# Kernel optimization log

Hardware: AMD Instinct MI355X
Metric: run time of the kernel (lower is better)

## Reference

```python
import jax, jax.numpy as jnp
import numpy as np

B, N, D = 4, 2048, 1024
WIN, K, ALPHA = 4, 8, 0.3


def setup_inputs() -> dict:
    key = jax.random.key(0)
    ks = jax.random.split(key, 16)
    s_d = 1.0 / np.sqrt(D)
    s_2d = 1.0 / np.sqrt(2 * D)
    inp = {
        'mu': jax.random.normal(ks[0], (B, N, D), jnp.float32),
        'pheromone': jax.random.uniform(ks[1], (B, N), jnp.float32),
        'Wq': jax.random.normal(ks[2], (D, D), jnp.float32) * s_d,
        'bq': jnp.zeros((D,), jnp.float32),
        'Wk': jax.random.normal(ks[3], (D, D), jnp.float32) * s_d,
        'bk': jnp.zeros((D,), jnp.float32),
        'Wv': jax.random.normal(ks[4], (D, D), jnp.float32) * s_d,
        'bv': jnp.zeros((D,), jnp.float32),
        'Wm1': jax.random.normal(ks[5], (2 * D, D), jnp.float32) * s_2d,
        'bm1': jnp.zeros((D,), jnp.float32),
        'Wm2': jax.random.normal(ks[6], (D, D), jnp.float32) * s_d,
        'bm2': jnp.zeros((D,), jnp.float32),
        'Wo': jax.random.normal(ks[7], (2 * D, D), jnp.float32) * s_2d,
        'bo': jnp.zeros((D,), jnp.float32),
    }
    return inp


def reference(mu, pheromone, Wq, bq, Wk, bk, Wv, bv, Wm1, bm1, Wm2, bm2, Wo, bo):
    # ---- local windowed gather-MLP ----
    padded = jnp.pad(mu, ((0, 0), (WIN, 0), (0, 0)))  # causal left-pad
    neighbors = jnp.stack([padded[:, WIN - w:WIN - w + N, :] for w in range(1, WIN + 1)], axis=2)
    self_exp = jnp.broadcast_to(mu[:, :, None, :], neighbors.shape)
    cat = jnp.concatenate([self_exp, neighbors], axis=-1)
    h = jax.nn.silu(cat @ Wm1 + bm1) @ Wm2 + bm2
    local_msgs = h.mean(axis=2)  # (B,N,D)

    # ---- causal top-k attention with pheromone bias ----
    q = mu @ Wq + bq
    k = mu @ Wk + bk
    v = mu @ Wv + bv
    scale = 1.0 / jnp.sqrt(jnp.asarray(D, mu.dtype))
    scores = jnp.einsum('bnd,bmd->bnm', q, k) * scale  # (B,N,N)
    scores = scores + ALPHA * pheromone[:, None, :]
    row = jnp.arange(N)
    causal = jnp.where(row[None, :] > row[:, None], -jnp.inf, 0.0).astype(mu.dtype)
    scores = scores + causal[None]
    # top-k sparsification (N > K): softmax over the k kept scores, zeros elsewhere
    vals, idx = jax.lax.top_k(scores, K)  # (B,N,K)
    probs = jax.nn.softmax(vals, axis=-1)
    bi = jnp.arange(B)[:, None, None]
    ni = jnp.arange(N)[None, :, None]
    attn = jnp.zeros_like(scores).at[bi, ni, idx].set(probs)
    global_msgs = jnp.einsum('bnm,bmd->bnd', attn, v)

    return jnp.concatenate([local_msgs, global_msgs], axis=-1) @ Wo + bo
```

## Files before the change

kernel.cpp:

```cpp
#include <hip/hip_runtime.h>
#include <hip/hip_bf16.h>
#include <math.h>

#define B_ 4
#define N_ 2048
#define D_ 1024
#define WIN_ 4
#define KTOP 8
#define ALPHA_ 0.3f
#define SCALE_ (1.0f/32.0f)
#define NCH 16
#define TROW 36

typedef unsigned short ushortT;
typedef __attribute__((ext_vector_type(8))) short short8v;
typedef __attribute__((ext_vector_type(4))) float f32x4;

__device__ inline ushortT f2b(float f) {
    unsigned int u = __float_as_uint(f);
    unsigned int r = (u + 0x7fffu + ((u >> 16) & 1u)) >> 16;
    return (ushortT)r;
}
__device__ inline float b2f(ushortT u) {
    return __uint_as_float(((unsigned int)u) << 16);
}

__global__ __launch_bounds__(256)
void split3_mu(const float* __restrict__ src, ushortT* __restrict__ Pa,
               ushortT* __restrict__ Pb, ushortT* __restrict__ CCbase)
{
    size_t base = ((size_t)blockIdx.x * 256 + threadIdx.x) * 4;
    int row = (int)(base >> 10);
    int col = (int)(base & 1023);
    float4 v = *reinterpret_cast<const float4*>(&src[base]);
    ushort4 pa, pb, pc;
    float vv[4] = {v.x, v.y, v.z, v.w};
#pragma unroll
    for (int j = 0; j < 4; ++j) {
        float f = vv[j];
        ushortT a = f2b(f);  float r1 = f - b2f(a);
        ushortT b = f2b(r1); float r2 = r1 - b2f(b);
        ushortT c = f2b(r2);
        ((ushortT*)&pa)[j] = a; ((ushortT*)&pb)[j] = b; ((ushortT*)&pc)[j] = c;
    }
    *reinterpret_cast<ushort4*>(&Pa[base]) = pa;
    *reinterpret_cast<ushort4*>(&Pb[base]) = pb;
    *reinterpret_cast<ushort4*>(&CCbase[(size_t)row * 2048 + 1024 + col]) = pc;
}

__global__ __launch_bounds__(256)
void transpose_f2b(const float* __restrict__ W, ushortT* __restrict__ Wt,
                   int K, int Nn)
{
    __shared__ float t[32][33];
    const int k0 = blockIdx.x * 32, n0 = blockIdx.y * 32;
    const int tx = threadIdx.x & 31, ty8 = threadIdx.x >> 5;
#pragma unroll
    for (int p = 0; p < 4; ++p) {
        int kk = p * 8 + ty8;
        t[kk][tx] = W[(size_t)(k0 + kk) * Nn + n0 + tx];
    }
    __syncthreads();
#pragma unroll
    for (int p = 0; p < 4; ++p) {
        int nn = p * 8 + ty8;
        Wt[(size_t)(n0 + nn) * K + k0 + tx] = f2b(t[tx][nn]);
    }
}

__global__ __launch_bounds__(256)
void transpose_split3(const float* __restrict__ W, ushortT* __restrict__ Pa,
                      ushortT* __restrict__ Pb, ushortT* __restrict__ Pc,
                      int K, int Nn)
{
    __shared__ float t[32][33];
    const int k0 = blockIdx.x * 32, n0 = blockIdx.y * 32;
    const int tx = threadIdx.x & 31, ty8 = threadIdx.x >> 5;
#pragma unroll
    for (int p = 0; p < 4; ++p) {
        int kk = p * 8 + ty8;
        t[kk][tx] = W[(size_t)(k0 + kk) * Nn + n0 + tx];
    }
    __syncthreads();
#pragma unroll
    for (int p = 0; p < 4; ++p) {
        int nn = p * 8 + ty8;
        float f = t[tx][nn];
        ushortT a = f2b(f);  float r1 = f - b2f(a);
        ushortT b = f2b(r1); float r2 = r1 - b2f(b);
        ushortT c = f2b(r2);
        size_t o = (size_t)(n0 + nn) * K + k0 + tx;
        Pa[o] = a; Pb[o] = b; Pc[o] = c;
    }
}

template<int BF16OUT>
__global__ __launch_bounds__(256)
void mfma_gemm(const ushortT* __restrict__ A, int lda,
               const ushortT* __restrict__ Bt, int ldb,
               const float* __restrict__ bias,
               void* __restrict__ Cout, int ldc, int K)
{
    __shared__ ushortT AsL[128 * 72];
    __shared__ ushortT BsL[128 * 72];
    const int tid = threadIdx.x;
    const int m0 = blockIdx.y * 128;
    const int n0 = blockIdx.x * 128;
    const int w = tid >> 6, lane = tid & 63;
    const int wr = w >> 1, wc = w & 1;

    f32x4 acc[4][4];
#pragma unroll
    for (int mi = 0; mi < 4; ++mi)
#pragma unroll
        for (int ni = 0; ni < 4; ++ni) acc[mi][ni] = (f32x4){0.f, 0.f, 0.f, 0.f};

    for (int k0 = 0; k0 < K; k0 += 64) {
#pragma unroll
        for (int it = 0; it < 4; ++it) {
            int idx = tid + it * 256;
            int row = idx >> 3, c = idx & 7;
            int4 va = *reinterpret_cast<const int4*>(&A[(size_t)(m0 + row) * lda + k0 + c * 8]);
            *reinterpret_cast<int4*>(&AsL[row * 72 + c * 8]) = va;
            int4 vb = *reinterpret_cast<const int4*>(&Bt[(size_t)(n0 + row) * ldb + k0 + c * 8]);
            *reinterpret_cast<int4*>(&BsL[row * 72 + c * 8]) = vb;
        }
        __syncthreads();
#pragma unroll
        for (int kh = 0; kh < 2; ++kh) {
            const int ko = kh * 32 + (lane >> 4) * 8;
            const int rr = lane & 15;
            short8v af[4], bf[4];
#pragma unroll
            for (int mi = 0; mi < 4; ++mi)
                af[mi] = *reinterpret_cast<const short8v*>(&AsL[(wr * 64 + mi * 16 + rr) * 72 + ko]);
#pragma unroll
            for (int ni = 0; ni < 4; ++ni)
                bf[ni] = *reinterpret_cast<const short8v*>(&BsL[(wc * 64 + ni * 16 + rr) * 72 + ko]);
#pragma unroll
            for (int mi = 0; mi < 4; ++mi)
#pragma unroll
                for (int ni = 0; ni < 4; ++ni)
                    acc[mi][ni] = __builtin_amdgcn_mfma_f32_16x16x32_bf16(
                        af[mi], bf[ni], acc[mi][ni], 0, 0, 0);
        }
        __syncthreads();
    }

    const int r4 = (lane >> 4) * 4, cl = lane & 15;
#pragma unroll
    for (int mi = 0; mi < 4; ++mi)
#pragma unroll
        for (int ni = 0; ni < 4; ++ni) {
            int row = m0 + wr * 64 + mi * 16 + r4;
            int col = n0 + wc * 64 + ni * 16 + cl;
            float bb = bias ? bias[col] : 0.f;
#pragma unroll
            for (int r = 0; r < 4; ++r) {
                float v = acc[mi][ni][r] + bb;
                if (BF16OUT)
                    ((ushortT*)Cout)[(size_t)(row + r) * ldc + col] = f2b(v);
                else
                    ((float*)Cout)[(size_t)(row + r) * ldc + col] = v;
            }
        }
}

__global__ __launch_bounds__(256)
void silu_mean(const float* __restrict__ A, const float* __restrict__ Nb,
               ushortT* __restrict__ Sb)
{
    size_t idx4 = (size_t)blockIdx.x * blockDim.x + threadIdx.x;
    size_t base = idx4 << 2;
    int n = (int)((base >> 10) & (N_ - 1));
    float4 a = *reinterpret_cast<const float4*>(&A[base]);
    float sx = 0.f, sy = 0.f, sz = 0.f, sw = 0.f;
#pragma unroll
    for (int w = 1; w <= WIN_; ++w) {
        float xx = a.x, xy = a.y, xz = a.z, xw = a.w;
        if (n >= w) {
            const float4 nb = *reinterpret_cast<const float4*>(&Nb[base - (size_t)w * D_]);
            xx += nb.x; xy += nb.y; xz += nb.z; xw += nb.w;
        }
        sx += xx / (1.f + __expf(-xx));
        sy += xy / (1.f + __expf(-xy));
        sz += xz / (1.f + __expf(-xz));
        sw += xw / (1.f + __expf(-xw));
    }
    ushort4 o = {f2b(sx * 0.25f), f2b(sy * 0.25f), f2b(sz * 0.25f), f2b(sw * 0.25f)};
    *reinterpret_cast<ushort4*>(&Sb[base]) = o;
}

__device__ inline void topk_insert(float (&tv)[KTOP], int (&ti)[KTOP], float s, int m)
{
    if ((s > tv[KTOP-1]) || (s == tv[KTOP-1] && m < ti[KTOP-1])) {
        float cs = s; int ci = m;
#pragma unroll
        for (int q = 0; q < KTOP; ++q) {
            bool beats = (cs > tv[q]) || (cs == tv[q] && ci < ti[q]);
            if (beats) { float t0 = tv[q]; int t1 = ti[q];
                         tv[q] = cs; ti[q] = ci; cs = t0; ci = t1; }
        }
    }
}

#define SPLIT6_COMPUTE(T6, wr, wc, lane, acc)                                   \
    {                                                                           \
        const int rr_ = (lane) & 15, ko_ = ((lane) >> 4) * 8;                   \
        _Pragma("unroll")                                                       \
        for (int p_ = 0; p_ < 3; ++p_) {                                        \
            short8v aF_[4];                                                     \
            _Pragma("unroll")                                                   \
            for (int mi_ = 0; mi_ < 4; ++mi_)                                   \
                aF_[mi_] = *reinterpret_cast<const short8v*>(                   \
                    &T6[p_ * 4608 + ((wr) * 64 + mi_ * 16 + rr_) * TROW + ko_]);\
            _Pragma("unroll")                                                   \
            for (int q_ = 0; q_ < 3; ++q_) {                                    \
                if (p_ + q_ > 2) continue;                                      \
                short8v b0_ = *reinterpret_cast<const short8v*>(                \
                    &T6[(3 + q_) * 4608 + ((wc) * 32 + rr_) * TROW + ko_]);     \
                short8v b1_ = *reinterpret_cast<const short8v*>(                \
                    &T6[(3 + q_) * 4608 + ((wc) * 32 + 16 + rr_) * TROW + ko_]);\
                _Pragma("unroll")                                               \
                for (int mi_ = 0; mi_ < 4; ++mi_) {                             \
                    acc[mi_][0] = __builtin_amdgcn_mfma_f32_16x16x32_bf16(      \
                        aF_[mi_], b0_, acc[mi_][0], 0, 0, 0);                   \
                    acc[mi_][1] = __builtin_amdgcn_mfma_f32_16x16x32_bf16(      \
                        aF_[mi_], b1_, acc[mi_][1], 0, 0, 0);                   \
                }                                                               \
            }                                                                   \
        }                                                                       \
    }

__global__ __launch_bounds__(512, 4)
void gemm_split6(const ushortT* __restrict__ A0, const ushortT* __restrict__ A1,
                 const ushortT* __restrict__ A2, int lda, int ldac,
                 const ushortT* __restrict__ B0, const ushortT* __restrict__ B1,
                 const ushortT* __restrict__ B2,
                 const float* __restrict__ bias,
                 ushortT* __restrict__ Pa, ushortT* __restrict__ Pb,
                 ushortT* __restrict__ Pc)
{
    __shared__ ushortT T6[6 * 128 * TROW];

    int lin = blockIdx.y * 8 + blockIdx.x;
    lin = (lin & 7) * 64 + (lin >> 3);
    const int m0 = (lin >> 3) * 128;
    const int n0 = (lin & 7) * 128;

    const int tid = threadIdx.x;
    const int wid = tid >> 6, lane = tid & 63;
    const int wr = wid >> 2, wc = wid & 3;
    const int rowL = tid >> 2, cL = tid & 3;

    const size_t offA  = (size_t)(m0 + rowL) * lda + cL * 8;
    const size_t offAc = (size_t)(m0 + rowL) * ldac + cL * 8;
    const size_t offB  = (size_t)(n0 + rowL) * D_ + cL * 8;
    const int ldst = rowL * TROW + cL * 8;

    f32x4 acc[4][2];
#pragma unroll
    for (int mi = 0; mi < 4; ++mi) { acc[mi][0] = (f32x4){0,0,0,0}; acc[mi][1] = (f32x4){0,0,0,0}; }

    int4 s0, s1, s2, s3, s4, s5;
    s0 = *reinterpret_cast<const int4*>(&A0[offA]);
    s1 = *reinterpret_cast<const int4*>(&A1[offA]);
    s2 = *reinterpret_cast<const int4*>(&A2[offAc]);
    s3 = *reinterpret_cast<const int4*>(&B0[offB]);
    s4 = *reinterpret_cast<const int4*>(&B1[offB]);
    s5 = *reinterpret_cast<const int4*>(&B2[offB]);

    for (int ks = 0; ks < 32; ++ks) {
        __syncthreads();
        *reinterpret_cast<int4*>(&T6[0 * 4608 + ldst]) = s0;
        *reinterpret_cast<int4*>(&T6[1 * 4608 + ldst]) = s1;
        *reinterpret_cast<int4*>(&T6[2 * 4608 + ldst]) = s2;
        *reinterpret_cast<int4*>(&T6[3 * 4608 + ldst]) = s3;
        *reinterpret_cast<int4*>(&T6[4 * 4608 + ldst]) = s4;
        *reinterpret_cast<int4*>(&T6[5 * 4608 + ldst]) = s5;
        __syncthreads();
        if (ks < 31) {
            const int kk = (ks + 1) * 32;
            s0 = *reinterpret_cast<const int4*>(&A0[offA + kk]);
            s1 = *reinterpret_cast<const int4*>(&A1[offA + kk]);
            s2 = *reinterpret_cast<const int4*>(&A2[offAc + kk]);
            s3 = *reinterpret_cast<const int4*>(&B0[offB + kk]);
            s4 = *reinterpret_cast<const int4*>(&B1[offB + kk]);
            s5 = *reinterpret_cast<const int4*>(&B2[offB + kk]);
        }
        SPLIT6_COMPUTE(T6, wr, wc, lane, acc)
    }

    const int r4 = (lane >> 4) * 4, cl = lane & 15;
#pragma unroll
    for (int mi = 0; mi < 4; ++mi)
#pragma unroll
        for (int ni = 0; ni < 2; ++ni) {
            int col = n0 + wc * 32 + ni * 16 + cl;
            float bb = bias[col];
#pragma unroll
            for (int r = 0; r < 4; ++r) {
                int row = m0 + wr * 64 + mi * 16 + r4 + r;
                float v = acc[mi][ni][r] + bb;
                ushortT a = f2b(v);  float r1 = v - b2f(a);
                ushortT b = f2b(r1); float r2 = r1 - b2f(b);
                ushortT c = f2b(r2);
                size_t o = (size_t)row * D_ + col;
                Pa[o] = a; Pb[o] = b; Pc[o] = c;
            }
        }
}

__global__ __launch_bounds__(512, 4)
void attn_scores_mfma2(const ushortT* __restrict__ Qa, const ushortT* __restrict__ Qb2,
                       const ushortT* __restrict__ Qc,
                       const ushortT* __restrict__ Ka, const ushortT* __restrict__ Kb2,
                       const ushortT* __restrict__ Kc,
                       const float* __restrict__ pher,
                       float* __restrict__ WV, int* __restrict__ WI)
{
    __shared__ ushortT T6[6 * 128 * TROW];
    __shared__ float Ps[128];
    float* MV = reinterpret_cast<float*>(&T6[0]);
    int*   MI = reinterpret_cast<int*>((char*)&T6[0] + 16384);
    float* PV = reinterpret_cast<float*>((char*)&T6[0] + 32768);
    int*   PI = reinterpret_cast<int*>((char*)&T6[0] + 36864);

    int lin = blockIdx.y * 136 + blockIdx.x;
    lin = (lin & 7) * 68 + (lin >> 3);
    const int b = lin / 136;
    const int xy = lin - b * 136;
    int g = 0;
    while ((g + 1) * (g + 2) / 2 <= xy) ++g;
    const int ch = xy - g * (g + 1) / 2;
    const int n0 = g * 128;
    const int m0 = ch * 128;
    const size_t bN = (size_t)b * N_;

    const int tid = threadIdx.x;
    const int wid = tid >> 6, lane = tid & 63;
    const int wr = wid >> 2, wc = wid & 3;
    const int rowL = tid >> 2, cL = tid & 3;

    if (tid < 128) Ps[tid] = pher[bN + m0 + tid];

    const size_t offQ = (bN + n0 + rowL) * (size_t)D_ + cL * 8;
    const size_t offK = (bN + m0 + rowL) * (size_t)D_ + cL * 8;
    const int ldst = rowL * TROW + cL * 8;

    f32x4 acc[4][2];
#pragma unroll
    for (int mi = 0; mi < 4; ++mi) { acc[mi][0] = (f32x4){0,0,0,0}; acc[mi][1] = (f32x4){0,0,0,0}; }

    int4 s0, s1, s2, s3, s4, s5;
    s0 = *reinterpret_cast<const int4*>(&Qa[offQ]);
    s1 = *reinterpret_cast<const int4*>(&Qb2[offQ]);
    s2 = *reinterpret_cast<const int4*>(&Qc[offQ]);
    s3 = *reinterpret_cast<const int4*>(&Ka[offK]);
    s4 = *reinterpret_cast<const int4*>(&Kb2[offK]);
    s5 = *reinterpret_cast<const int4*>(&Kc[offK]);

    for (int ks = 0; ks < 32; ++ks) {
        __syncthreads();
        *reinterpret_cast<int4*>(&T6[0 * 4608 + ldst]) = s0;
        *reinterpret_cast<int4*>(&T6[1 * 4608 + ldst]) = s1;
        *reinterpret_cast<int4*>(&T6[2 * 4608 + ldst]) = s2;
        *reinterpret_cast<int4*>(&T6[3 * 4608 + ldst]) = s3;
        *reinterpret_cast<int4*>(&T6[4 * 4608 + ldst]) = s4;
        *reinterpret_cast<int4*>(&T6[5 * 4608 + ldst]) = s5;
        __syncthreads();
        if (ks < 31) {
            const int kk = (ks + 1) * 32;
            s0 = *reinterpret_cast<const int4*>(&Qa[offQ + kk]);
            s1 = *reinterpret_cast<const int4*>(&Qb2[offQ + kk]);
            s2 = *reinterpret_cast<const int4*>(&Qc[offQ + kk]);
            s3 = *reinterpret_cast<const int4*>(&Ka[offK + kk]);
            s4 = *reinterpret_cast<const int4*>(&Kb2[offK + kk]);
            s5 = *reinterpret_cast<const int4*>(&Kc[offK + kk]);
        }
        SPLIT6_COMPUTE(T6, wr, wc, lane, acc)
    }

    const int r4 = (lane >> 4) * 4, cl = lane & 15;
    for (int p = 0; p < 4; ++p) {
        __syncthreads();
        if (wr == (p >> 1)) {
#pragma unroll
            for (int mi2 = 0; mi2 < 2; ++mi2) {
                const int mi = (p & 1) * 2 + mi2;
#pragma unroll
                for (int ni = 0; ni < 2; ++ni) {
                    int col = wc * 32 + ni * 16 + cl;
                    int m = m0 + col;
#pragma unroll
                    for (int r = 0; r < 4; ++r) {
                        int rloc = mi2 * 16 + r4 + r;
                        int n = n0 + p * 32 + rloc;
                        bool ok = (m <= n);
                        MV[rloc * 128 + col] = ok ? (acc[mi][ni][r] * SCALE_ + ALPHA_ * Ps[col])
                                                  : -INFINITY;
                        MI[rloc * 128 + col] = ok ? m : 0x7fffffff;
                    }
                }
            }
        }
        __syncthreads();
        if (tid < 128) {
            const int row = tid >> 2, q4 = tid & 3;
            float tv[KTOP]; int ti[KTOP];
#pragma unroll
            for (int j = 0; j < KTOP; ++j) { tv[j] = -INFINITY; ti[j] = 0x7fffffff; }
            for (int j = 0; j < 32; ++j) {
                float s = MV[row * 128 + q4 * 32 + j];
                if (s == -INFINITY) continue;
                topk_insert(tv, ti, s, MI[row * 128 + q4 * 32 + j]);
            }
#pragma unroll
            for (int j = 0; j < KTOP; ++j) {
                PV[(row * 4 + q4) * 8 + j] = tv[j];
                PI[(row * 4 + q4) * 8 + j] = ti[j];
            }
        }
        __syncthreads();
        if (tid < 32) {
            float tv[KTOP]; int ti[KTOP];
#pragma unroll
            for (int j = 0; j < KTOP; ++j) { tv[j] = -INFINITY; ti[j] = 0x7fffffff; }
            for (int i = 0; i < 32; ++i) {
                float s = PV[tid * 32 + i];
                if (s == -INFINITY) continue;
                topk_insert(tv, ti, s, PI[tid * 32 + i]);
            }
            int n = n0 + p * 32 + tid;
            size_t base = ((bN + n) * NCH + ch) * 8;
#pragma unroll
            for (int j = 0; j < KTOP; ++j) { WV[base + j] = tv[j]; WI[base + j] = ti[j]; }
        }
    }
}

__global__ __launch_bounds__(256)
void attn_merge(const float* __restrict__ WV, const int* __restrict__ WI,
                const ushortT* __restrict__ V, ushortT* __restrict__ CCb)
{
    __shared__ float CV[4][128];
    __shared__ int   CI[4][128];
    __shared__ float Pp[4][KTOP];
    __shared__ int   Pi[4][KTOP];

    const int tid  = threadIdx.x;
    const int wv   = tid >> 6;
    const int lane = tid & 63;
    const int rid  = blockIdx.x * 4 + wv;
    const int b    = rid >> 11;
    const int n    = rid & (N_ - 1);
    const int ncand = ((n >> 7) + 1) * 8;
    const size_t cbase = (size_t)rid * (NCH * 8);

#pragma unroll
    for (int t = 0; t < 2; ++t) {
        int i = lane + t * 64;
        if (i < ncand) { CV[wv][i] = WV[cbase + i]; CI[wv][i] = WI[cbase + i]; }
        else           { CV[wv][i] = -INFINITY;     CI[wv][i] = 0x7fffffff;   }
    }
    __syncthreads();

    if (lane == 0) {
        float tv[KTOP]; int ti[KTOP];
#pragma unroll
        for (int j = 0; j < KTOP; ++j) { tv[j] = -INFINITY; ti[j] = 0x7fffffff; }
        for (int i = 0; i < 128; ++i) {
            float s = CV[wv][i];
            if (s == -INFINITY) continue;
            topk_insert(tv, ti, s, CI[wv][i]);
        }
        float mx = tv[0];
        float e[KTOP]; float sum = 0.f;
#pragma unroll
        for (int j = 0; j < KTOP; ++j) {
            e[j] = (tv[j] == -INFINITY) ? 0.f : __expf(tv[j] - mx);
            sum += e[j];
        }
        float inv = 1.f / sum;
#pragma unroll
        for (int j = 0; j < KTOP; ++j) {
            Pp[wv][j] = e[j] * inv;
            Pi[wv][j] = (tv[j] == -INFINITY) ? 0 : ti[j];
        }
    }
    __syncthreads();

    const size_t vbase = (size_t)b * N_ * D_;
#pragma unroll
    for (int it = 0; it < 2; ++it) {
        int c8 = (it * 64 + lane) * 8;
        float o[8];
#pragma unroll
        for (int u = 0; u < 8; ++u) o[u] = 0.f;
#pragma unroll
        for (int j = 0; j < KTOP; ++j) {
            float p = Pp[wv][j];
            ushort4 v0 = *reinterpret_cast<const ushort4*>(
                &V[vbase + (size_t)Pi[wv][j] * D_ + c8]);
            ushort4 v1 = *reinterpret_cast<const ushort4*>(
                &V[vbase + (size_t)Pi[wv][j] * D_ + c8 + 4]);
            o[0] = fmaf(p, b2f(v0.x), o[0]); o[1] = fmaf(p, b2f(v0.y), o[1]);
            o[2] = fmaf(p, b2f(v0.z), o[2]); o[3] = fmaf(p, b2f(v0.w), o[3]);
            o[4] = fmaf(p, b2f(v1.x), o[4]); o[5] = fmaf(p, b2f(v1.y), o[5]);
            o[6] = fmaf(p, b2f(v1.z), o[6]); o[7] = fmaf(p, b2f(v1.w), o[7]);
        }
        ushort4 ob0 = {f2b(o[0]), f2b(o[1]), f2b(o[2]), f2b(o[3])};
        ushort4 ob1 = {f2b(o[4]), f2b(o[5]), f2b(o[6]), f2b(o[7])};
        *reinterpret_cast<ushort4*>(&CCb[(size_t)rid * 2048 + 1024 + c8]) = ob0;
        *reinterpret_cast<ushort4*>(&CCb[(size_t)rid * 2048 + 1024 + c8 + 4]) = ob1;
    }
}

extern "C" void kernel_launch(void* const* d_in, const int* in_sizes, int n_in,
                              void* d_out, int out_size, void* d_ws, size_t ws_size,
                              hipStream_t stream)
{
    const float* mu   = (const float*)d_in[0];
    const float* pher = (const float*)d_in[1];
    const float* Wq   = (const float*)d_in[2];
    const float* bq   = (const float*)d_in[3];
    const float* Wk   = (const float*)d_in[4];
    const float* bk   = (const float*)d_in[5];
    const float* Wv   = (const float*)d_in[6];
    const float* bv   = (const float*)d_in[7];
    const float* Wm1  = (const float*)d_in[8];
    const float* bm1  = (const float*)d_in[9];
    const float* Wm2  = (const float*)d_in[10];
    const float* bm2  = (const float*)d_in[11];
    const float* Wo   = (const float*)d_in[12];
    const float* bo   = (const float*)d_in[13];
    float* out = (float*)d_out;
    float* ws  = (float*)d_ws;

    const size_t SZ  = (size_t)B_ * N_ * D_;
    const size_t MEG = 1024 * 1024;
    const int M = B_ * N_;

    ushortT* CCb   = (ushortT*)ws;
    ushortT* mu_cp = CCb + 1024;
    float*   AbF   = ws + SZ;
    ushortT* Qa    = (ushortT*)(ws + SZ);
    ushortT* Qb2   = Qa + SZ;
    float*   NbF   = ws + 2 * SZ;
    ushortT* Ka    = (ushortT*)(ws + 2 * SZ);
    ushortT* Kb2   = Ka + SZ;
    ushortT* mu_a  = (ushortT*)(ws + 3 * SZ);
    ushortT* mu_bp = (ushortT*)(ws + 3 * SZ + SZ / 2);
    float*   WVb   = (float*)(ws + 3 * SZ + SZ / 2);
    int*     WIb   = (int*)(WVb + MEG);
    ushortT* U     = (ushortT*)(ws + 4 * SZ);
    ushortT* Wt_m1 = U;
    ushortT* Wt_m2 = U + 2 * MEG;
    ushortT* Wt_v  = U + 3 * MEG;
    ushortT* WqT_a = U;            ushortT* WqT_b = U + MEG;     ushortT* WqT_c = U + 2 * MEG;
    ushortT* WkT_a = U + 3 * MEG;  ushortT* WkT_b = U + 4 * MEG; ushortT* WkT_c = U + 5 * MEG;
    ushortT* Wt_o  = U;
    ushortT* Vb16  = (ushortT*)(ws + 4 * SZ + 3 * MEG);
    ushortT* SbB   = (ushortT*)(ws + 4 * SZ + 3 * MEG + SZ / 2);
    ushortT* Qc    = SbB;
    ushortT* Kc    = (ushortT*)(ws + 4 * SZ + 3 * MEG + SZ);

    dim3 blk256(256), blk512(512);
    dim3 gD(8, 64);

    hipLaunchKernelGGL(split3_mu, dim3(SZ / 4 / 256), blk256, 0, stream, mu, mu_a, mu_bp, CCb);
    hipLaunchKernelGGL(transpose_f2b, dim3(64, 32), blk256, 0, stream, Wm1, Wt_m1, 2048, 1024);
    hipLaunchKernelGGL(transpose_f2b, dim3(32, 32), blk256, 0, stream, Wm2, Wt_m2, 1024, 1024);
    hipLaunchKernelGGL(transpose_f2b, dim3(32, 32), blk256, 0, stream, Wv, Wt_v, 1024, 1024);
    hipLaunchKernelGGL((mfma_gemm<0>), gD, blk256, 0, stream,
                       mu_a, D_, Wt_m1, 2048, bm1, (void*)AbF, D_, D_);
    hipLaunchKernelGGL((mfma_gemm<0>), gD, blk256, 0, stream,
                       mu_a, D_, Wt_m1 + 1024, 2048, (const float*)nullptr, (void*)NbF, D_, D_);
    hipLaunchKernelGGL(silu_mean, dim3(SZ / 4 / 256), blk256, 0, stream, AbF, NbF, SbB);
    hipLaunchKernelGGL((mfma_gemm<1>), gD, blk256, 0, stream,
                       SbB, D_, Wt_m2, D_, bm2, (void*)CCb, 2 * D_, D_);
    hipLaunchKernelGGL((mfma_gemm<1>), gD, blk256, 0, stream,
                       mu_a, D_, Wt_v, D_, bv, (void*)Vb16, D_, D_);
    hipLaunchKernelGGL(transpose_split3, dim3(32, 32), blk256, 0, stream,
                       Wq, WqT_a, WqT_b, WqT_c, 1024, 1024);
    hipLaunchKernelGGL(transpose_split3, dim3(32, 32), blk256, 0, stream,
                       Wk, WkT_a, WkT_b, WkT_c, 1024, 1024);
    hipLaunchKernelGGL(gemm_split6, gD, blk512, 0, stream,
                       mu_a, mu_bp, mu_cp, D_, 2 * D_,
                       WqT_a, WqT_b, WqT_c, bq, Qa, Qb2, Qc);
    hipLaunchKernelGGL(gemm_split6, gD, blk512, 0, stream,
                       mu_a, mu_bp, mu_cp, D_, 2 * D_,
                       WkT_a, WkT_b, WkT_c, bk, Ka, Kb2, Kc);
    hipLaunchKernelGGL(transpose_f2b, dim3(64, 32), blk256, 0, stream, Wo, Wt_o, 2048, 1024);
    hipLaunchKernelGGL(attn_scores_mfma2, dim3(136, B_), blk512, 0, stream,
                       Qa, Qb2, Qc, Ka, Kb2, Kc, pher, WVb, WIb);
    hipLaunchKernelGGL(attn_merge, dim3(M / 4), blk256, 0, stream, WVb, WIb, Vb16, CCb);
    hipLaunchKernelGGL((mfma_gemm<0>), gD, blk256, 0, stream,
                       CCb, 2 * D_, Wt_o, 2048, bo, (void*)out, D_, 2 * D_);

    (void)in_sizes; (void)n_in; (void)out_size; (void)ws_size;
}
```

Before: 896.1 us.

## Use 64x64 per-wave tiles with 256-thread blocks in split6 GEMM and scores

Both split-precision MFMA kernels (gemm_split6 and attn_scores_mfma2) move from 8 waves with 64x32 wave tiles to 4 waves with 64x64 wave tiles. Each thread now stages two 16-byte chunks per operand per k-step. The compute loop loads all three A-split fragments once and reuses each B fragment across four MFMA columns, which cuts LDS reads per MFMA. The cost is more accumulator and fragment registers per thread (launch bounds 256,2) and fewer waves to hide latency. The top-k epilogue must still be correct with half the threads.

```diff
diff --git a/kernel.cpp b/kernel.cpp
--- a/kernel.cpp
+++ b/kernel.cpp
@@ -204,35 +204,62 @@
     }
 }
 
-#define SPLIT6_COMPUTE(T6, wr, wc, lane, acc)                                   \
+#define SPLIT6_COMPUTE64(T6, wr, wc, lane, acc)                                 \
     {                                                                           \
         const int rr_ = (lane) & 15, ko_ = ((lane) >> 4) * 8;                   \
+        short8v aF_[3][4];                                                      \
         _Pragma("unroll")                                                       \
         for (int p_ = 0; p_ < 3; ++p_) {                                        \
-            short8v aF_[4];                                                     \
             _Pragma("unroll")                                                   \
             for (int mi_ = 0; mi_ < 4; ++mi_)                                   \
-                aF_[mi_] = *reinterpret_cast<const short8v*>(                   \
+                aF_[p_][mi_] = *reinterpret_cast<const short8v*>(               \
                     &T6[p_ * 4608 + ((wr) * 64 + mi_ * 16 + rr_) * TROW + ko_]);\
+        }                                                                       \
+        _Pragma("unroll")                                                       \
+        for (int q_ = 0; q_ < 3; ++q_) {                                        \
+            short8v bF_[4];                                                     \
             _Pragma("unroll")                                                   \
-            for (int q_ = 0; q_ < 3; ++q_) {                                    \
-                if (p_ + q_ > 2) continue;                                      \
-                short8v b0_ = *reinterpret_cast<const short8v*>(                \
-                    &T6[(3 + q_) * 4608 + ((wc) * 32 + rr_) * TROW + ko_]);     \
-                short8v b1_ = *reinterpret_cast<const short8v*>(                \
-                    &T6[(3 + q_) * 4608 + ((wc) * 32 + 16 + rr_) * TROW + ko_]);\
+            for (int ni_ = 0; ni_ < 4; ++ni_)                                   \
+                bF_[ni_] = *reinterpret_cast<const short8v*>(                   \
+                    &T6[(3 + q_) * 4608 + ((wc) * 64 + ni_ * 16 + rr_) * TROW + ko_]); \
+            _Pragma("unroll")                                                   \
+            for (int p_ = 0; p_ < 3 - q_; ++p_) {                               \
                 _Pragma("unroll")                                               \
-                for (int mi_ = 0; mi_ < 4; ++mi_) {                             \
-                    acc[mi_][0] = __builtin_amdgcn_mfma_f32_16x16x32_bf16(      \
-                        aF_[mi_], b0_, acc[mi_][0], 0, 0, 0);                   \
-                    acc[mi_][1] = __builtin_amdgcn_mfma_f32_16x16x32_bf16(      \
-                        aF_[mi_], b1_, acc[mi_][1], 0, 0, 0);                   \
-                }                                                               \
+                for (int mi_ = 0; mi_ < 4; ++mi_)                               \
+                    _Pragma("unroll")                                           \
+                    for (int ni_ = 0; ni_ < 4; ++ni_)                           \
+                        acc[mi_][ni_] = __builtin_amdgcn_mfma_f32_16x16x32_bf16(\
+                            aF_[p_][mi_], bF_[ni_], acc[mi_][ni_], 0, 0, 0);    \
             }                                                                   \
         }                                                                       \
     }
 
-__global__ __launch_bounds__(512, 4)
+#define SPLIT6_LOAD(sreg, P0, P1, P2, P3, P4, P5, oA, oAc, oB, kk)              \
+    {                                                                           \
+        sreg[0][0] = *reinterpret_cast<const int4*>(&P0[oA + (kk)]);            \
+        sreg[0][1] = *reinterpret_cast<const int4*>(&P0[oA + (kk) + 8]);        \
+        sreg[1][0] = *reinterpret_cast<const int4*>(&P1[oA + (kk)]);            \
+        sreg[1][1] = *reinterpret_cast<const int4*>(&P1[oA + (kk) + 8]);        \
+        sreg[2][0] = *reinterpret_cast<const int4*>(&P2[oAc + (kk)]);           \
+        sreg[2][1] = *reinterpret_cast<const int4*>(&P2[oAc + (kk) + 8]);       \
+        sreg[3][0] = *reinterpret_cast<const int4*>(&P3[oB + (kk)]);            \
+        sreg[3][1] = *reinterpret_cast<const int4*>(&P3[oB + (kk) + 8]);        \
+        sreg[4][0] = *reinterpret_cast<const int4*>(&P4[oB + (kk)]);            \
+        sreg[4][1] = *reinterpret_cast<const int4*>(&P4[oB + (kk) + 8]);        \
+        sreg[5][0] = *reinterpret_cast<const int4*>(&P5[oB + (kk)]);            \
+        sreg[5][1] = *reinterpret_cast<const int4*>(&P5[oB + (kk) + 8]);        \
+    }
+
+#define SPLIT6_STORE(sreg, ldst)                                                \
+    {                                                                           \
+        _Pragma("unroll")                                                       \
+        for (int t_ = 0; t_ < 6; ++t_) {                                        \
+            *reinterpret_cast<int4*>(&T6[t_ * 4608 + (ldst)]) = sreg[t_][0];    \
+            *reinterpret_cast<int4*>(&T6[t_ * 4608 + (ldst) + 8]) = sreg[t_][1];\
+        }                                                                       \
+    }
+
+__global__ __launch_bounds__(256, 2)
 void gemm_split6(const ushortT* __restrict__ A0, const ushortT* __restrict__ A1,
                  const ushortT* __restrict__ A2, int lda, int ldac,
                  const ushortT* __restrict__ B0, const ushortT* __restrict__ B1,
@@ -250,53 +277,41 @@
 
     const int tid = threadIdx.x;
     const int wid = tid >> 6, lane = tid & 63;
-    const int wr = wid >> 2, wc = wid & 3;
-    const int rowL = tid >> 2, cL = tid & 3;
-
-    const size_t offA  = (size_t)(m0 + rowL) * lda + cL * 8;
-    const size_t offAc = (size_t)(m0 + rowL) * ldac + cL * 8;
-    const size_t offB  = (size_t)(n0 + rowL) * D_ + cL * 8;
-    const int ldst = rowL * TROW + cL * 8;
-
-    f32x4 acc[4][2];
-#pragma unroll
-    for (int mi = 0; mi < 4; ++mi) { acc[mi][0] = (f32x4){0,0,0,0}; acc[mi][1] = (f32x4){0,0,0,0}; }
-
-    int4 s0, s1, s2, s3, s4, s5;
-    s0 = *reinterpret_cast<const int4*>(&A0[offA]);
-    s1 = *reinterpret_cast<const int4*>(&A1[offA]);
-    s2 = *reinterpret_cast<const int4*>(&A2[offAc]);
-    s3 = *reinterpret_cast<const int4*>(&B0[offB]);
-    s4 = *reinterpret_cast<const int4*>(&B1[offB]);
-    s5 = *reinterpret_cast<const int4*>(&B2[offB]);
+    const int wr = wid >> 1, wc = wid & 1;
+    const int rowL = tid >> 1;
+    const int cL2  = (tid & 1) * 16;
+
+    const size_t offA  = (size_t)(m0 + rowL) * lda + cL2;
+    const size_t offAc = (size_t)(m0 + rowL) * ldac + cL2;
+    const size_t offB  = (size_t)(n0 + rowL) * D_ + cL2;
+    const int ldst = rowL * TROW + cL2;
+
+    f32x4 acc[4][4];
+#pragma unroll
+    for (int mi = 0; mi < 4; ++mi)
+#pragma unroll
+        for (int ni = 0; ni < 4; ++ni) acc[mi][ni] = (f32x4){0,0,0,0};
+
+    int4 s[6][2];
+    SPLIT6_LOAD(s, A0, A1, A2, B0, B1, B2, offA, offAc, offB, 0)
 
     for (int ks = 0; ks < 32; ++ks) {
         __syncthreads();
-        *reinterpret_cast<int4*>(&T6[0 * 4608 + ldst]) = s0;
-        *reinterpret_cast<int4*>(&T6[1 * 4608 + ldst]) = s1;
-        *reinterpret_cast<int4*>(&T6[2 * 4608 + ldst]) = s2;
-        *reinterpret_cast<int4*>(&T6[3 * 4608 + ldst]) = s3;
-        *reinterpret_cast<int4*>(&T6[4 * 4608 + ldst]) = s4;
-        *reinterpret_cast<int4*>(&T6[5 * 4608 + ldst]) = s5;
+        SPLIT6_STORE(s, ldst)
         __syncthreads();
         if (ks < 31) {
             const int kk = (ks + 1) * 32;
-            s0 = *reinterpret_cast<const int4*>(&A0[offA + kk]);
-            s1 = *reinterpret_cast<const int4*>(&A1[offA + kk]);
-            s2 = *reinterpret_cast<const int4*>(&A2[offAc + kk]);
-            s3 = *reinterpret_cast<const int4*>(&B0[offB + kk]);
-            s4 = *reinterpret_cast<const int4*>(&B1[offB + kk]);
-            s5 = *reinterpret_cast<const int4*>(&B2[offB + kk]);
-        }
-        SPLIT6_COMPUTE(T6, wr, wc, lane, acc)
+            SPLIT6_LOAD(s, A0, A1, A2, B0, B1, B2, offA, offAc, offB, kk)
+        }
+        SPLIT6_COMPUTE64(T6, wr, wc, lane, acc)
     }
 
     const int r4 = (lane >> 4) * 4, cl = lane & 15;
 #pragma unroll
     for (int mi = 0; mi < 4; ++mi)
 #pragma unroll
-        for (int ni = 0; ni < 2; ++ni) {
-            int col = n0 + wc * 32 + ni * 16 + cl;
+        for (int ni = 0; ni < 4; ++ni) {
+            int col = n0 + wc * 64 + ni * 16 + cl;
             float bb = bias[col];
 #pragma unroll
             for (int r = 0; r < 4; ++r) {
@@ -311,7 +326,7 @@
         }
 }
 
-__global__ __launch_bounds__(512, 4)
+__global__ __launch_bounds__(256, 2)
 void attn_scores_mfma2(const ushortT* __restrict__ Qa, const ushortT* __restrict__ Qb2,
                        const ushortT* __restrict__ Qc,
                        const ushortT* __restrict__ Ka, const ushortT* __restrict__ Kb2,
@@ -339,46 +354,34 @@
 
     const int tid = threadIdx.x;
     const int wid = tid >> 6, lane = tid & 63;
-    const int wr = wid >> 2, wc = wid & 3;
-    const int rowL = tid >> 2, cL = tid & 3;
+    const int wr = wid >> 1, wc = wid & 1;
+    const int rowL = tid >> 1;
+    const int cL2  = (tid & 1) * 16;
 
     if (tid < 128) Ps[tid] = pher[bN + m0 + tid];
 
-    const size_t offQ = (bN + n0 + rowL) * (size_t)D_ + cL * 8;
-    const size_t offK = (bN + m0 + rowL) * (size_t)D_ + cL * 8;
-    const int ldst = rowL * TROW + cL * 8;
-
-    f32x4 acc[4][2];
-#pragma unroll
-    for (int mi = 0; mi < 4; ++mi) { acc[mi][0] = (f32x4){0,0,0,0}; acc[mi][1] = (f32x4){0,0,0,0}; }
-
-    int4 s0, s1, s2, s3, s4, s5;
-    s0 = *reinterpret_cast<const int4*>(&Qa[offQ]);
-    s1 = *reinterpret_cast<const int4*>(&Qb2[offQ]);
-    s2 = *reinterpret_cast<const int4*>(&Qc[offQ]);
-    s3 = *reinterpret_cast<const int4*>(&Ka[offK]);
-    s4 = *reinterpret_cast<const int4*>(&Kb2[offK]);
-    s5 = *reinterpret_cast<const int4*>(&Kc[offK]);
+    const size_t offQ = (bN + n0 + rowL) * (size_t)D_ + cL2;
+    const size_t offK = (bN + m0 + rowL) * (size_t)D_ + cL2;
+    const int ldst = rowL * TROW + cL2;
+
+    f32x4 acc[4][4];
+#pragma unroll
+    for (int mi = 0; mi < 4; ++mi)
+#pragma unroll
+        for (int ni = 0; ni < 4; ++ni) acc[mi][ni] = (f32x4){0,0,0,0};
+
+    int4 s[6][2];
+    SPLIT6_LOAD(s, Qa, Qb2, Qc, Ka, Kb2, Kc, offQ, offQ, offK, 0)
 
     for (int ks = 0; ks < 32; ++ks) {
         __syncthreads();
-        *reinterpret_cast<int4*>(&T6[0 * 4608 + ldst]) = s0;
-        *reinterpret_cast<int4*>(&T6[1 * 4608 + ldst]) = s1;
-        *reinterpret_cast<int4*>(&T6[2 * 4608 + ldst]) = s2;
-        *reinterpret_cast<int4*>(&T6[3 * 4608 + ldst]) = s3;
-        *reinterpret_cast<int4*>(&T6[4 * 4608 + ldst]) = s4;
-        *reinterpret_cast<int4*>(&T6[5 * 4608 + ldst]) = s5;
+        SPLIT6_STORE(s, ldst)
         __syncthreads();
         if (ks < 31) {
             const int kk = (ks + 1) * 32;
-            s0 = *reinterpret_cast<const int4*>(&Qa[offQ + kk]);
-            s1 = *reinterpret_cast<const int4*>(&Qb2[offQ + kk]);
-            s2 = *reinterpret_cast<const int4*>(&Qc[offQ + kk]);
-            s3 = *reinterpret_cast<const int4*>(&Ka[offK + kk]);
-            s4 = *reinterpret_cast<const int4*>(&Kb2[offK + kk]);
-            s5 = *reinterpret_cast<const int4*>(&Kc[offK + kk]);
-        }
-        SPLIT6_COMPUTE(T6, wr, wc, lane, acc)
+            SPLIT6_LOAD(s, Qa, Qb2, Qc, Ka, Kb2, Kc, offQ, offQ, offK, kk)
+        }
+        SPLIT6_COMPUTE64(T6, wr, wc, lane, acc)
     }
 
     const int r4 = (lane >> 4) * 4, cl = lane & 15;
@@ -389,8 +392,8 @@
             for (int mi2 = 0; mi2 < 2; ++mi2) {
                 const int mi = (p & 1) * 2 + mi2;
 #pragma unroll
-                for (int ni = 0; ni < 2; ++ni) {
-                    int col = wc * 32 + ni * 16 + cl;
+                for (int ni = 0; ni < 4; ++ni) {
+                    int col = wc * 64 + ni * 16 + cl;
                     int m = m0 + col;
 #pragma unroll
                     for (int r = 0; r < 4; ++r) {
@@ -411,9 +414,9 @@
 #pragma unroll
             for (int j = 0; j < KTOP; ++j) { tv[j] = -INFINITY; ti[j] = 0x7fffffff; }
             for (int j = 0; j < 32; ++j) {
-                float s = MV[row * 128 + q4 * 32 + j];
-                if (s == -INFINITY) continue;
-                topk_insert(tv, ti, s, MI[row * 128 + q4 * 32 + j]);
+                float s2 = MV[row * 128 + q4 * 32 + j];
+                if (s2 == -INFINITY) continue;
+                topk_insert(tv, ti, s2, MI[row * 128 + q4 * 32 + j]);
             }
 #pragma unroll
             for (int j = 0; j < KTOP; ++j) {
@@ -427,9 +430,9 @@
 #pragma unroll
             for (int j = 0; j < KTOP; ++j) { tv[j] = -INFINITY; ti[j] = 0x7fffffff; }
             for (int i = 0; i < 32; ++i) {
-                float s = PV[tid * 32 + i];
-                if (s == -INFINITY) continue;
-                topk_insert(tv, ti, s, PI[tid * 32 + i]);
+                float s2 = PV[tid * 32 + i];
+                if (s2 == -INFINITY) continue;
+                topk_insert(tv, ti, s2, PI[tid * 32 + i]);
             }
             int n = n0 + p * 32 + tid;
             size_t base = ((bN + n) * NCH + ch) * 8;
@@ -565,7 +568,7 @@
     ushortT* Qc    = SbB;
     ushortT* Kc    = (ushortT*)(ws + 4 * SZ + 3 * MEG + SZ);
 
-    dim3 blk256(256), blk512(512);
+    dim3 blk256(256);
     dim3 gD(8, 64);
 
     hipLaunchKernelGGL(split3_mu, dim3(SZ / 4 / 256), blk256, 0, stream, mu, mu_a, mu_bp, CCb);
@@ -585,14 +588,14 @@
                        Wq, WqT_a, WqT_b, WqT_c, 1024, 1024);
     hipLaunchKernelGGL(transpose_split3, dim3(32, 32), blk256, 0, stream,
                        Wk, WkT_a, WkT_b, WkT_c, 1024, 1024);
-    hipLaunchKernelGGL(gemm_split6, gD, blk512, 0, stream,
+    hipLaunchKernelGGL(gemm_split6, gD, blk256, 0, stream,
                        mu_a, mu_bp, mu_cp, D_, 2 * D_,
                        WqT_a, WqT_b, WqT_c, bq, Qa, Qb2, Qc);
-    hipLaunchKernelGGL(gemm_split6, gD, blk512, 0, stream,
+    hipLaunchKernelGGL(gemm_split6, gD, blk256, 0, stream,
                        mu_a, mu_bp, mu_cp, D_, 2 * D_,
                        WkT_a, WkT_b, WkT_c, bk, Ka, Kb2, Kc);
     hipLaunchKernelGGL(transpose_f2b, dim3(64, 32), blk256, 0, stream, Wo, Wt_o, 2048, 1024);
-    hipLaunchKernelGGL(attn_scores_mfma2, dim3(136, B_), blk512, 0, stream,
+    hipLaunchKernelGGL(attn_scores_mfma2, dim3(136, B_), blk256, 0, stream,
                        Qa, Qb2, Qc, Ka, Kb2, Kc, pher, WVb, WIb);
     hipLaunchKernelGGL(attn_merge, dim3(M / 4), blk256, 0, stream, WVb, WIb, Vb16, CCb);
     hipLaunchKernelGGL((mfma_gemm<0>), gD, blk256, 0, stream,
```

Result: slower. 2.034 ms (+127.0%).
